# Kernel tuning notes

Hardware: AMD Instinct MI355X
Metric: run time of the kernel (lower is better)

The kernel has to match this reference:

```python
import jax, jax.numpy as jnp
import numpy as np

H = 16
EMB = 1024
DH = 64  # att_dim


def setup_inputs() -> dict:
    key = jax.random.key(0)
    k1, k2, k3 = jax.random.split(key, 3)
    B, T = 4, 2048
    x = jax.random.normal(k1, (B, T, EMB), dtype=jnp.float32)
    # torch nn.Linear weight layout: [out_features, in_features]
    w_qkv = jax.random.normal(k2, (3 * H * DH, EMB), dtype=jnp.float32) * (1.0 / np.sqrt(EMB))
    wo = jax.random.normal(k3, (EMB, H * DH), dtype=jnp.float32) * (1.0 / np.sqrt(H * DH))
    return {"x": x, "w_qkv": w_qkv, "wo": wo}


def reference(x, w_qkv, wo):
    B, T, C = x.shape
    qkv = jnp.einsum('btc,oc->bto', x, w_qkv)  # [B,T,3*H*DH]
    q, k, v = jnp.split(qkv, 3, axis=-1)
    # [B,H,T,DH]
    q = q.reshape(B, T, H, DH).transpose(0, 2, 1, 3)
    k = k.reshape(B, T, H, DH).transpose(0, 2, 1, 3)
    v = v.reshape(B, T, H, DH).transpose(0, 2, 1, 3)
    scale = 1.0 / np.sqrt(DH).astype(np.float32)
    scores = jnp.einsum('bhqd,bhkd->bhqk', q, k) * scale
    causal = jnp.tril(jnp.ones((T, T), dtype=bool))
    scores = jnp.where(causal, scores, jnp.finfo(scores.dtype).min)
    attn = jax.nn.softmax(scores, axis=-1)
    y = jnp.einsum('bhqk,bhkd->bhqd', attn, v)  # [B,H,T,DH]
    y = y.transpose(0, 2, 1, 3).reshape(B, T, H * DH)
    return jnp.einsum('bti,oi->bto', y, wo)
```

## Files before the change

### kernel.cpp

```cpp
#include <hip/hip_runtime.h>
#include <hip/hip_bf16.h>
#include <stdint.h>


typedef __attribute__((ext_vector_type(8))) short short8;
typedef __attribute__((ext_vector_type(4))) float floatx4;

extern "C" __device__ float __ocml_native_exp2_f32(float);

__device__ __forceinline__ ushort f2bf(float f) {
  uint32_t u = __float_as_uint(f);
  u += 0x7fff + ((u >> 16) & 1);
  return (ushort)(u >> 16);
}

#if __has_builtin(__builtin_amdgcn_cvt_pk_bf16_f32)
typedef __attribute__((ext_vector_type(2))) __bf16 bf16x2;
__device__ __forceinline__ uint32_t pack_bf16(float a, float b) {
  union { bf16x2 v; uint32_t u; } cv;
  cv.v = __builtin_amdgcn_cvt_pk_bf16_f32(a, b);
  return cv.u;
}
#else
__device__ __forceinline__ uint32_t pack_bf16(float a, float b) {
  uint32_t ua = __float_as_uint(a) + 0x8000u;
  uint32_t ub = __float_as_uint(b) + 0x8000u;
  return __builtin_amdgcn_perm(ub, ua, 0x07060302u);
}
#endif

__device__ __forceinline__ void gload16(const ushort* g, ushort* l) {
  __builtin_amdgcn_global_load_lds(
      (const __attribute__((address_space(1))) void*)g,
      (__attribute__((address_space(3))) void*)l, 16, 0, 0);
}

__global__ __launch_bounds__(256) void cvt3_kernel(const float* __restrict__ x,
                                                   const float* __restrict__ wq,
                                                   const float* __restrict__ wo,
                                                   ushort* __restrict__ xo,
                                                   ushort* __restrict__ wqo,
                                                   ushort* __restrict__ woo) {
  int i = blockIdx.x * 256 + threadIdx.x;
  const float* in; ushort* out; int idx;
  if (i < 2097152)      { in = x;  out = xo;  idx = i; }
  else if (i < 2883584) { in = wq; out = wqo; idx = i - 2097152; }
  else                  { in = wo; out = woo; idx = i - 2883584; }
  float4 v = ((const float4*)in)[idx];
  ushort4 o;
  o.x = f2bf(v.x); o.y = f2bf(v.y); o.z = f2bf(v.z); o.w = f2bf(v.w);
  ((ushort4*)out)[idx] = o;
}

__global__ __launch_bounds__(512) void gemm256(const ushort* __restrict__ A,
                                               const ushort* __restrict__ Bw,
                                               ushort* __restrict__ qb,
                                               ushort* __restrict__ kb,
                                               ushort* __restrict__ vt) {
  constexpr int SLOT = 12288;
  __shared__ ushort ring[3 * SLOT];
  int tid = threadIdx.x;
  int lane = tid & 63, wave = tid >> 6;
  int lrow = lane & 15, quad = lane >> 4;
  int wm = wave >> 1, wn = wave & 1;
  int wm64 = wm * 64, wn64 = wn * 64;
  int m0 = blockIdx.x * 256, n0 = blockIdx.y * 128;

  int srow = tid >> 2;
  int schunk8 = ((tid & 3) ^ ((tid >> 3) & 3)) * 8;
  const ushort* Ag0 = A + (size_t)(m0 + srow) * 1024 + schunk8;
  const ushort* Ag1 = Ag0 + (size_t)128 * 1024;
  const ushort* Bg0 = Bw + (size_t)(n0 + srow) * 1024 + schunk8;
  int fo2 = (quad ^ ((lrow >> 1) & 3)) * 8;

  const floatx4 zero4 = {0.f, 0.f, 0.f, 0.f};
  floatx4 acc[4][4];
#pragma unroll
  for (int i = 0; i < 4; i++)
#pragma unroll
    for (int j = 0; j < 4; j++) acc[i][j] = zero4;

  auto stage = [&](int t) {
    ushort* Sa = &ring[(t % 3) * SLOT];
    size_t kk = (size_t)t * 32;
    gload16(Ag0 + kk, &Sa[wave * 16 * 32]);
    gload16(Ag1 + kk, &Sa[(128 + wave * 16) * 32]);
    gload16(Bg0 + kk, &Sa[8192 + wave * 16 * 32]);
  };

  short8 fAa[4], fAb[4], fBa[4], fBb[4];

#define READF(u_, FN)                                                         \
  {                                                                           \
    ushort* As_ = &ring[((u_) % 3) * SLOT];                                   \
    ushort* Bs_ = As_ + 8192;                                                 \
    _Pragma("unroll")                                                         \
    for (int mi = 0; mi < 4; mi++)                                            \
      FN##a[mi] = *(const short8*)(&As_[(wm64 + mi * 16 + lrow) * 32 + fo2]); \
    _Pragma("unroll")                                                         \
    for (int nj = 0; nj < 4; nj++)                                            \
      FN##b[nj] = *(const short8*)(&Bs_[(wn64 + nj * 16 + lrow) * 32 + fo2]); \
  }

#define MFMAS(FC)                                                             \
  {                                                                           \
    __builtin_amdgcn_s_setprio(1);                                            \
    _Pragma("unroll")                                                         \
    for (int mi = 0; mi < 4; mi++)                                            \
      _Pragma("unroll")                                                       \
      for (int nj = 0; nj < 4; nj++)                                          \
        acc[mi][nj] = __builtin_amdgcn_mfma_f32_16x16x32_bf16(                \
            FC##a[mi], FC##b[nj], acc[mi][nj], 0, 0, 0);                      \
    __builtin_amdgcn_s_setprio(0);                                            \
  }

#define BARRIER(N_)                                                           \
  asm volatile("s_waitcnt vmcnt(" #N_ ")" ::: "memory");                      \
  __builtin_amdgcn_s_barrier();                                               \
  asm volatile("" ::: "memory");

#define KITER(u_, N_, ISSUE_, FC, FN)                                         \
  {                                                                           \
    BARRIER(N_)                                                               \
    READF(u_, FN)                                                             \
    if (ISSUE_) stage((u_) + 2);                                              \
    MFMAS(FC)                                                                 \
  }

  stage(0); stage(1);
  BARRIER(3)
  READF(0, fA)
  stage(2);
#pragma unroll 1
  for (int p = 0; p < 14; ++p) {
    KITER(2 * p + 1, 3, true, fA, fB);
    KITER(2 * p + 2, 3, true, fB, fA);
  }
  KITER(29, 3, true, fA, fB);
  KITER(30, 3, false, fB, fA);
  KITER(31, 0, false, fA, fB);
  MFMAS(fB)

#undef KITER
#undef BARRIER
#undef MFMAS
#undef READF

  constexpr int CS = 136;
  ushort* sm = ring;
  int sec = n0 >> 10;
  int hrow = tid >> 4, kcol = tid & 15;
  __syncthreads();

  if (sec < 2) {
    float qs = (sec == 0) ? 0.18033688f : 1.0f;
    ushort* dst = (sec == 0) ? qb : kb;
    int hbase = n0 & 1023;
#pragma unroll 1
    for (int hf = 0; hf < 2; ++hf) {
      if ((wm >> 1) == hf) {
#pragma unroll
        for (int mi = 0; mi < 4; mi++)
#pragma unroll
          for (int nj = 0; nj < 4; nj++)
#pragma unroll
            for (int r = 0; r < 4; r++)
              sm[((wm & 1) * 64 + mi * 16 + quad * 4 + r) * CS +
                 wn64 + nj * 16 + lrow] = f2bf(acc[mi][nj][r] * qs);
      }
      __syncthreads();
#pragma unroll
      for (int mi = 0; mi < 4; mi++) {
        int mloc = mi * 32 + hrow;
        int m = m0 + hf * 128 + mloc, b_ = m >> 11, t = m & 2047;
        int col = kcol * 8;
        int h = (hbase + col) >> 6, d = col & 63;
        uint4 val = *(const uint4*)(&sm[mloc * CS + col]);
        *(uint4*)(dst + ((size_t)(b_ * 16 + h) * 2048 + t) * 64 + d) = val;
      }
      __syncthreads();
    }
  } else {
    int b_ = m0 >> 11, t0 = m0 & 2047;
#pragma unroll 1
    for (int hf = 0; hf < 2; ++hf) {
      if ((wm >> 1) == hf) {
#pragma unroll
        for (int mi = 0; mi < 4; mi++)
#pragma unroll
          for (int nj = 0; nj < 4; nj++) {
            uint2 w;
            w.x = pack_bf16(acc[mi][nj][0], acc[mi][nj][1]);
            w.y = pack_bf16(acc[mi][nj][2], acc[mi][nj][3]);
            *(uint2*)(&sm[(wn64 + nj * 16 + lrow) * CS +
                          (wm & 1) * 64 + mi * 16 + quad * 4]) = w;
          }
      }
      __syncthreads();
#pragma unroll
      for (int di = 0; di < 4; di++) {
        int nloc = di * 32 + hrow;
        int n = n0 + nloc, h = (n & 1023) >> 6, d = n & 63;
        uint4 val = *(const uint4*)(&sm[nloc * CS + kcol * 8]);
        *(uint4*)(vt + ((size_t)(b_ * 16 + h) * 64 + d) * 2048 +
                  t0 + hf * 128 + kcol * 8) = val;
      }
      __syncthreads();
    }
  }
}

__global__ __launch_bounds__(256) void gemm_bt(const ushort* __restrict__ A,
                                               const ushort* __restrict__ Bw,
                                               float* __restrict__ Cf) {
  __shared__ ushort smem[128 * 64 * 2];
  ushort* As = smem;
  ushort* Bs = smem + 128 * 64;
  int tid = threadIdx.x;
  int lane = tid & 63, wave = tid >> 6;
  int lrow = lane & 15, quad = lane >> 4;
  int wr = (wave >> 1) * 64, wc = (wave & 1) * 64;
  int m0 = blockIdx.x * 128, n0 = blockIdx.y * 128;

  const floatx4 zero4 = {0.f, 0.f, 0.f, 0.f};
  floatx4 acc[4][4];
#pragma unroll
  for (int i = 0; i < 4; i++)
#pragma unroll
    for (int j = 0; j < 4; j++) acc[i][j] = zero4;

  int rsub = tid >> 3;
  int colb = (((tid & 7) ^ (rsub & 7)) * 8);
  const ushort* Ag = A + (size_t)(m0 + rsub) * 1024 + colb;
  const ushort* Bg = Bw + (size_t)(n0 + rsub) * 1024 + colb;
  int fo = (quad ^ (lrow & 7)) * 8;

  for (int kk = 0; kk < 1024; kk += 64) {
    __syncthreads();
#pragma unroll
    for (int i = 0; i < 4; i++) {
      gload16(Ag + kk + (size_t)i * 32 * 1024, &As[(8 * wave + 32 * i) * 64]);
      gload16(Bg + kk + (size_t)i * 32 * 1024, &Bs[(8 * wave + 32 * i) * 64]);
    }
    __syncthreads();
#pragma unroll
    for (int ks = 0; ks < 2; ks++) {
      short8 a[4], b[4];
#pragma unroll
      for (int i = 0; i < 4; i++)
        a[i] = *(const short8*)(&As[(wr + i * 16 + lrow) * 64 + (fo ^ (32 * ks))]);
#pragma unroll
      for (int j = 0; j < 4; j++)
        b[j] = *(const short8*)(&Bs[(wc + j * 16 + lrow) * 64 + (fo ^ (32 * ks))]);
#pragma unroll
      for (int i = 0; i < 4; i++)
#pragma unroll
        for (int j = 0; j < 4; j++)
          acc[i][j] = __builtin_amdgcn_mfma_f32_16x16x32_bf16(a[i], b[j], acc[i][j], 0, 0, 0);
    }
  }

#pragma unroll
  for (int i = 0; i < 4; i++)
#pragma unroll
    for (int j = 0; j < 4; j++)
#pragma unroll
      for (int r = 0; r < 4; r++) {
        int m = m0 + wr + i * 16 + quad * 4 + r;
        int n = n0 + wc + j * 16 + lrow;
        Cf[(size_t)m * 1024 + n] = acc[i][j][r];
      }
}

__global__ __launch_bounds__(512) void attn_kernel(const ushort* __restrict__ qg,
                                                   const ushort* __restrict__ kg,
                                                   const ushort* __restrict__ vg,
                                                   ushort* __restrict__ y) {
  __shared__ ushort Ks[64 * 64];
  __shared__ ushort Vs[64 * 64];
  __shared__ ushort Ps[8 * 16 * 72];
  int tid = threadIdx.x;
  int lane = tid & 63, wave = tid >> 6;
  int lrow = lane & 15, quad = lane >> 4;
  int gx = blockIdx.x, gy = blockIdx.y;
  int pr = gy >> 3;
  int bh = (gy & 7) * 8 + gx;
  const ushort* qp = qg + (size_t)bh * 2048 * 64;
  const ushort* kp = kg + (size_t)bh * 2048 * 64;
  const ushort* vp = vg + (size_t)bh * 64 * 2048;
  int b = bh >> 4, h = bh & 15;
  int srow = tid >> 3, sc = tid & 7;
  int sswz = ((sc ^ (srow & 7)) * 8);
  int fo = (quad ^ (lrow & 7)) * 8;
  ushort* Pw = &Ps[wave * 16 * 72];

  const floatx4 zero4 = {0.f, 0.f, 0.f, 0.f};
  short8 ones;
#pragma unroll
  for (int i = 0; i < 8; i++) ones[i] = (short)0x3F80;

#pragma unroll 1
  for (int pass = 0; pass < 2; ++pass) {
    int qt = pass ? (15 - pr) : pr;
    int last = 2 * qt + 1;

    const ushort* qrow_p = qp + (size_t)((qt << 7) + wave * 16 + lrow) * 64;
    short8 a_q0 = *(const short8*)(qrow_p + quad * 8);
    short8 a_q1 = *(const short8*)(qrow_p + (quad ^ 4) * 8);

    uint4 kreg = *(const uint4*)(kp + (size_t)srow * 64 + sc * 8);
    uint4 vreg = *(const uint4*)(vp + (size_t)srow * 2048 + sc * 8);

    floatx4 l_acc = zero4;
    floatx4 o_acc[4];
#pragma unroll
    for (int j = 0; j < 4; j++) o_acc[j] = zero4;

#pragma unroll 1
    for (int kv = 0; kv <= last; kv++) {
      __syncthreads();
      *(uint4*)(&Ks[srow * 64 + sswz]) = kreg;
      *(uint4*)(&Vs[srow * 64 + sswz]) = vreg;
      if (kv < last) {
        kreg = *(const uint4*)(kp + (size_t)((kv + 1) * 64 + srow) * 64 + sc * 8);
        vreg = *(const uint4*)(vp + (size_t)srow * 2048 + (kv + 1) * 64 + sc * 8);
      }
      __syncthreads();

      floatx4 s[4];
#pragma unroll
      for (int ct = 0; ct < 4; ct++) {
        short8 k0 = *(const short8*)(&Ks[(ct * 16 + lrow) * 64 + fo]);
        short8 k1 = *(const short8*)(&Ks[(ct * 16 + lrow) * 64 + (fo ^ 32)]);
        floatx4 z = zero4;
        z = __builtin_amdgcn_mfma_f32_16x16x32_bf16(k0, a_q0, z, 0, 0, 0);
        z = __builtin_amdgcn_mfma_f32_16x16x32_bf16(k1, a_q1, z, 0, 0, 0);
        s[ct] = z;
      }

      if (kv >= 2 * qt) {
        int qabs = (qt << 7) + wave * 16 + lrow;
        int kbase = (kv << 6) + quad * 4;
#pragma unroll
        for (int ct = 0; ct < 4; ct++)
#pragma unroll
          for (int r = 0; r < 4; r++)
            if (kbase + ct * 16 + r > qabs) s[ct][r] = -1e30f;
      }

#pragma unroll
      for (int ct = 0; ct < 4; ct++) {
        float p0 = __ocml_native_exp2_f32(s[ct][0]);
        float p1 = __ocml_native_exp2_f32(s[ct][1]);
        float p2 = __ocml_native_exp2_f32(s[ct][2]);
        float p3 = __ocml_native_exp2_f32(s[ct][3]);
        uint2 w;
        w.x = pack_bf16(p0, p1);
        w.y = pack_bf16(p2, p3);
        *(uint2*)(&Pw[lrow * 72 + ct * 16 + quad * 4]) = w;
      }
      asm volatile("" ::: "memory");

      short8 a_p0 = *(const short8*)(&Pw[lrow * 72 + quad * 8]);
      short8 a_p1 = *(const short8*)(&Pw[lrow * 72 + 32 + quad * 8]);
      l_acc = __builtin_amdgcn_mfma_f32_16x16x32_bf16(a_p0, ones, l_acc, 0, 0, 0);
      l_acc = __builtin_amdgcn_mfma_f32_16x16x32_bf16(a_p1, ones, l_acc, 0, 0, 0);
#pragma unroll
      for (int j = 0; j < 4; j++) {
        short8 v0 = *(const short8*)(&Vs[(j * 16 + lrow) * 64 + fo]);
        short8 v1 = *(const short8*)(&Vs[(j * 16 + lrow) * 64 + (fo ^ 32)]);
        o_acc[j] = __builtin_amdgcn_mfma_f32_16x16x32_bf16(a_p0, v0, o_acc[j], 0, 0, 0);
        o_acc[j] = __builtin_amdgcn_mfma_f32_16x16x32_bf16(a_p1, v1, o_acc[j], 0, 0, 0);
      }
    }

    float inv[4];
#pragma unroll
    for (int r = 0; r < 4; r++) inv[r] = 1.0f / l_acc[r];

#pragma unroll
    for (int j = 0; j < 4; j++)
#pragma unroll
      for (int r = 0; r < 4; r++) {
        int t = (qt << 7) + wave * 16 + quad * 4 + r;
        y[((size_t)b * 2048 + t) * 1024 + h * 64 + j * 16 + lrow] =
            f2bf(o_acc[j][r] * inv[r]);
      }
  }
}

extern "C" void kernel_launch(void* const* d_in, const int* in_sizes, int n_in,
                              void* d_out, int out_size, void* d_ws, size_t ws_size,
                              hipStream_t stream) {
  const float* x     = (const float*)d_in[0];
  const float* w_qkv = (const float*)d_in[1];
  const float* wo    = (const float*)d_in[2];
  float* out = (float*)d_out;

  ushort* x_bf    = (ushort*)d_ws;
  ushort* wqkv_bf = x_bf + (size_t)8192 * 1024;
  ushort* wo_bf   = wqkv_bf + (size_t)3072 * 1024;
  ushort* qb      = wo_bf + (size_t)1024 * 1024;
  ushort* kb      = qb + (size_t)8388608;
  ushort* vt      = kb + (size_t)8388608;
  ushort* yb      = x_bf;

  cvt3_kernel<<<12288, 256, 0, stream>>>(x, w_qkv, wo, x_bf, wqkv_bf, wo_bf);
  gemm256<<<dim3(32, 24), 512, 0, stream>>>(x_bf, wqkv_bf, qb, kb, vt);
  attn_kernel<<<dim3(8, 64), 512, 0, stream>>>(qb, kb, vt, yb);
  gemm_bt<<<dim3(64, 8), 256, 0, stream>>>(yb, wo_bf, out);
}
```

Before: 224.8 us.

## Pipeline output GEMM with triple-buffered LDS ring and relax attention barriers

The output projection GEMM is rewritten to use a 3-slot shared-memory ring with 32-wide K steps. Each step prefetches two stages ahead, double-buffers register fragments, and raises wave priority around the MFMA block, so global loads overlap with matrix math instead of being serialized behind a barrier. The attention kernel's __syncthreads calls are replaced by raw s_barrier with explicit waitcnt, which drops the implicit vmcnt wait so the prefetched K/V global loads stay in flight across the barrier. This relies on careful manual waitcnt counts, and getting them wrong would produce races.

```diff
diff --git a/kernel.cpp b/kernel.cpp
--- a/kernel.cpp
+++ b/kernel.cpp
@@ -210,18 +210,25 @@
   }
 }
 
-__global__ __launch_bounds__(256) void gemm_bt(const ushort* __restrict__ A,
-                                               const ushort* __restrict__ Bw,
-                                               float* __restrict__ Cf) {
-  __shared__ ushort smem[128 * 64 * 2];
-  ushort* As = smem;
-  ushort* Bs = smem + 128 * 64;
+__global__ __launch_bounds__(256) void gemm_out(const ushort* __restrict__ A,
+                                                const ushort* __restrict__ Bw,
+                                                float* __restrict__ Cf) {
+  constexpr int SLOT = 8192;
+  __shared__ ushort ring[3 * SLOT];
   int tid = threadIdx.x;
   int lane = tid & 63, wave = tid >> 6;
   int lrow = lane & 15, quad = lane >> 4;
   int wr = (wave >> 1) * 64, wc = (wave & 1) * 64;
   int m0 = blockIdx.x * 128, n0 = blockIdx.y * 128;
 
+  int srow = tid >> 2;
+  int schunk8 = ((tid & 3) ^ ((tid >> 3) & 3)) * 8;
+  const ushort* Ag0 = A + (size_t)(m0 + srow) * 1024 + schunk8;
+  const ushort* Ag1 = Ag0 + (size_t)64 * 1024;
+  const ushort* Bg0 = Bw + (size_t)(n0 + srow) * 1024 + schunk8;
+  const ushort* Bg1 = Bg0 + (size_t)64 * 1024;
+  int fo2 = (quad ^ ((lrow >> 1) & 3)) * 8;
+
   const floatx4 zero4 = {0.f, 0.f, 0.f, 0.f};
   floatx4 acc[4][4];
 #pragma unroll
@@ -229,46 +236,82 @@
 #pragma unroll
     for (int j = 0; j < 4; j++) acc[i][j] = zero4;
 
-  int rsub = tid >> 3;
-  int colb = (((tid & 7) ^ (rsub & 7)) * 8);
-  const ushort* Ag = A + (size_t)(m0 + rsub) * 1024 + colb;
-  const ushort* Bg = Bw + (size_t)(n0 + rsub) * 1024 + colb;
-  int fo = (quad ^ (lrow & 7)) * 8;
-
-  for (int kk = 0; kk < 1024; kk += 64) {
-    __syncthreads();
-#pragma unroll
-    for (int i = 0; i < 4; i++) {
-      gload16(Ag + kk + (size_t)i * 32 * 1024, &As[(8 * wave + 32 * i) * 64]);
-      gload16(Bg + kk + (size_t)i * 32 * 1024, &Bs[(8 * wave + 32 * i) * 64]);
-    }
-    __syncthreads();
-#pragma unroll
-    for (int ks = 0; ks < 2; ks++) {
-      short8 a[4], b[4];
-#pragma unroll
-      for (int i = 0; i < 4; i++)
-        a[i] = *(const short8*)(&As[(wr + i * 16 + lrow) * 64 + (fo ^ (32 * ks))]);
-#pragma unroll
-      for (int j = 0; j < 4; j++)
-        b[j] = *(const short8*)(&Bs[(wc + j * 16 + lrow) * 64 + (fo ^ (32 * ks))]);
-#pragma unroll
-      for (int i = 0; i < 4; i++)
-#pragma unroll
-        for (int j = 0; j < 4; j++)
-          acc[i][j] = __builtin_amdgcn_mfma_f32_16x16x32_bf16(a[i], b[j], acc[i][j], 0, 0, 0);
-    }
-  }
-
-#pragma unroll
-  for (int i = 0; i < 4; i++)
-#pragma unroll
-    for (int j = 0; j < 4; j++)
+  auto stage = [&](int t) {
+    ushort* Sa = &ring[(t % 3) * SLOT];
+    size_t kk = (size_t)t * 32;
+    gload16(Ag0 + kk, &Sa[wave * 16 * 32]);
+    gload16(Ag1 + kk, &Sa[(64 + wave * 16) * 32]);
+    gload16(Bg0 + kk, &Sa[4096 + wave * 16 * 32]);
+    gload16(Bg1 + kk, &Sa[4096 + (64 + wave * 16) * 32]);
+  };
+
+  short8 fAa[4], fAb[4], fBa[4], fBb[4];
+
+#define READF(u_, FN)                                                         \
+  {                                                                           \
+    ushort* As_ = &ring[((u_) % 3) * SLOT];                                   \
+    ushort* Bs_ = As_ + 4096;                                                 \
+    _Pragma("unroll")                                                         \
+    for (int mi = 0; mi < 4; mi++)                                            \
+      FN##a[mi] = *(const short8*)(&As_[(wr + mi * 16 + lrow) * 32 + fo2]);   \
+    _Pragma("unroll")                                                         \
+    for (int nj = 0; nj < 4; nj++)                                            \
+      FN##b[nj] = *(const short8*)(&Bs_[(wc + nj * 16 + lrow) * 32 + fo2]);   \
+  }
+
+#define MFMAS(FC)                                                             \
+  {                                                                           \
+    __builtin_amdgcn_s_setprio(1);                                            \
+    _Pragma("unroll")                                                         \
+    for (int mi = 0; mi < 4; mi++)                                            \
+      _Pragma("unroll")                                                       \
+      for (int nj = 0; nj < 4; nj++)                                          \
+        acc[mi][nj] = __builtin_amdgcn_mfma_f32_16x16x32_bf16(                \
+            FC##a[mi], FC##b[nj], acc[mi][nj], 0, 0, 0);                      \
+    __builtin_amdgcn_s_setprio(0);                                            \
+  }
+
+#define BARRIER(N_)                                                           \
+  asm volatile("s_waitcnt vmcnt(" #N_ ")" ::: "memory");                      \
+  __builtin_amdgcn_s_barrier();                                               \
+  asm volatile("" ::: "memory");
+
+#define KITER(u_, N_, ISSUE_, FC, FN)                                         \
+  {                                                                           \
+    BARRIER(N_)                                                               \
+    READF(u_, FN)                                                             \
+    if (ISSUE_) stage((u_) + 2);                                              \
+    MFMAS(FC)                                                                 \
+  }
+
+  stage(0); stage(1);
+  BARRIER(4)
+  READF(0, fA)
+  stage(2);
+#pragma unroll 1
+  for (int p = 0; p < 14; ++p) {
+    KITER(2 * p + 1, 4, true, fA, fB);
+    KITER(2 * p + 2, 4, true, fB, fA);
+  }
+  KITER(29, 4, true, fA, fB);
+  KITER(30, 4, false, fB, fA);
+  KITER(31, 0, false, fA, fB);
+  MFMAS(fB)
+
+#undef KITER
+#undef BARRIER
+#undef MFMAS
+#undef READF
+
+#pragma unroll
+  for (int mi = 0; mi < 4; mi++)
+#pragma unroll
+    for (int nj = 0; nj < 4; nj++)
 #pragma unroll
       for (int r = 0; r < 4; r++) {
-        int m = m0 + wr + i * 16 + quad * 4 + r;
-        int n = n0 + wc + j * 16 + lrow;
-        Cf[(size_t)m * 1024 + n] = acc[i][j][r];
+        int m = m0 + wr + mi * 16 + quad * 4 + r;
+        int n = n0 + wc + nj * 16 + lrow;
+        Cf[(size_t)m * 1024 + n] = acc[mi][nj][r];
       }
 }
 
@@ -318,14 +361,18 @@
 
 #pragma unroll 1
     for (int kv = 0; kv <= last; kv++) {
-      __syncthreads();
+      asm volatile("" ::: "memory");
+      __builtin_amdgcn_s_barrier();
+      asm volatile("" ::: "memory");
       *(uint4*)(&Ks[srow * 64 + sswz]) = kreg;
       *(uint4*)(&Vs[srow * 64 + sswz]) = vreg;
       if (kv < last) {
         kreg = *(const uint4*)(kp + (size_t)((kv + 1) * 64 + srow) * 64 + sc * 8);
         vreg = *(const uint4*)(vp + (size_t)srow * 2048 + (kv + 1) * 64 + sc * 8);
       }
-      __syncthreads();
+      asm volatile("s_waitcnt lgkmcnt(0)" ::: "memory");
+      __builtin_amdgcn_s_barrier();
+      asm volatile("" ::: "memory");
 
       floatx4 s[4];
 #pragma unroll
@@ -408,5 +455,5 @@
   cvt3_kernel<<<12288, 256, 0, stream>>>(x, w_qkv, wo, x_bf, wqkv_bf, wo_bf);
   gemm256<<<dim3(32, 24), 512, 0, stream>>>(x_bf, wqkv_bf, qb, kb, vt);
   attn_kernel<<<dim3(8, 64), 512, 0, stream>>>(qb, kb, vt, yb);
-  gemm_bt<<<dim3(64, 8), 256, 0, stream>>>(yb, wo_bf, out);
-}
+  gemm_out<<<dim3(64, 8), 256, 0, stream>>>(yb, wo_bf, out);
+}
```

Result: faster. 218.7 us (-2.7%).
